# Optimization experiments

Hardware: AMD Instinct MI355X
Metric: run time of the kernel (lower is better)

## Reference

```python
import jax, jax.numpy as jnp
import numpy as np

N, L, DV, EF = 64, 128, 16, 4
D, H, FF, LC, K, MS = 256, 8, 1024, 3, 6, 16
DK = D // H
NEG = -1e9


def _ln(x, g, b):
    m = x.mean(-1, keepdims=True)
    v = ((x - m) ** 2).mean(-1, keepdims=True)
    return (x - m) / jnp.sqrt(v + 1e-5) * g + b


def setup_inputs() -> dict:
    key = jax.random.key(0)
    ks = jax.random.split(key, 20)
    s = 0.05
    rn = lambda k, sh: jax.random.normal(k, sh, jnp.float32) * s
    return {
        "vehicles": jax.random.normal(ks[0], (N, L, DV), jnp.float32),
        "fleet_edges": jax.random.uniform(ks[1], (N, L, L, EF), jnp.float32),
        "Wproj": rn(ks[2], (DV, D)), "bproj": jnp.zeros((D,), jnp.float32),
        "Wq": rn(ks[3], (LC, D, D)), "Wk": rn(ks[4], (LC, D, D)), "Wv": rn(ks[5], (LC, D, D)),
        "mix1_w": rn(ks[6], (LC, H, 2, MS)), "mix1_b": jnp.zeros((LC, H, MS), jnp.float32),
        "mix2_w": rn(ks[7], (LC, H, MS)), "mix2_b": jnp.zeros((LC, H), jnp.float32),
        "Wo": rn(ks[8], (LC, D, D)), "bo": jnp.zeros((LC, D), jnp.float32),
        "n1_g": jnp.ones((LC, D), jnp.float32), "n1_b": jnp.zeros((LC, D), jnp.float32),
        "ff1_w": rn(ks[9], (LC, D, FF)), "ff1_b": jnp.zeros((LC, FF), jnp.float32),
        "ff2_w": rn(ks[10], (LC, FF, D)), "ff2_b": jnp.zeros((LC, D), jnp.float32),
        "n2_g": jnp.ones((LC, D), jnp.float32), "n2_b": jnp.zeros((LC, D), jnp.float32),
    }


def _forward(vehicles, fleet_edges, Wproj, bproj, Wq, Wk, Wv, mix1_w, mix1_b,
             mix2_w, mix2_b, Wo, bo, n1_g, n1_b, ff1_w, ff1_b, ff2_w, ff2_b, n2_g, n2_b):
    h = vehicles @ Wproj + bproj                      # (N, L, D)
    dist = fleet_edges[..., 0]                        # (N, L, L)
    cost = dist
    # kNN mask: keep K smallest distances per row; mask==True -> blocked
    _, knn_idx = jax.lax.top_k(-dist, K)              # (N, L, K)
    nbr = jnp.any(jax.nn.one_hot(knn_idx, L, dtype=bool), axis=2)  # (N, L, L)
    mask = ~nbr
    row_fully_masked = mask.all(-1)                   # (N, L)
    inv_sqrt_dk = 1.0 / np.sqrt(DK).astype(np.float32)
    for i in range(LC):
        q = (h @ Wq[i]).reshape(N, L, H, DK).transpose(0, 2, 1, 3)
        k_ = (h @ Wk[i]).reshape(N, L, H, DK).transpose(0, 2, 1, 3)
        v = (h @ Wv[i]).reshape(N, L, H, DK).transpose(0, 2, 1, 3)
        dot = jnp.einsum('nhrd,nhcd->nhrc', q, k_) * inv_sqrt_dk      # (N,H,L,L)
        cost_b = jnp.broadcast_to(cost[:, None], (N, H, L, L))
        two = jnp.stack([dot, cost_b], axis=-1)                        # (N,H,L,L,2)
        ms1 = jax.nn.relu(jnp.einsum('nhrct,htm->nhrcm', two, mix1_w[i])
                          + mix1_b[i][None, :, None, None, :])         # (N,H,L,L,MS)
        score = jnp.einsum('nhrcm,hm->nhrc', ms1, mix2_w[i]) \
                + mix2_b[i][None, :, None, None]                       # (N,H,L,L)
        score = jnp.where(mask[:, None], NEG, score)
        w = jax.nn.softmax(score, axis=-1)
        att = jnp.einsum('nhrc,nhcd->nhrd', w, v)
        att = att.transpose(0, 2, 1, 3).reshape(N, L, D) @ Wo[i] + bo[i]
        h1 = _ln(h + att, n1_g[i], n1_b[i])
        ff = jax.nn.relu(h1 @ ff1_w[i] + ff1_b[i]) @ ff2_w[i] + ff2_b[i]
        h = _ln(h1 + ff, n2_g[i], n2_b[i])
        # original does h_out[mask] = 0; with kNN k>0 every row keeps k entries,
        # so only fully-masked rows would be zeroed (a no-op here, kept for fidelity)
        h = jnp.where(row_fully_masked[..., None], 0.0, h)
    return h


def reference(vehicles, fleet_edges, Wproj, bproj, Wq, Wk, Wv, mix1_w, mix1_b,
              mix2_w, mix2_b, Wo, bo, n1_g, n1_b, ff1_w, ff1_b, ff2_w, ff2_b, n2_g, n2_b):
    return _forward(vehicles, fleet_edges, Wproj, bproj, Wq, Wk, Wv, mix1_w, mix1_b,
                    mix2_w, mix2_b, Wo, bo, n1_g, n1_b, ff1_w, ff1_b, ff2_w, ff2_b, n2_g, n2_b)
```

## Files before the change

kernel.cpp:

```cpp
#include <hip/hip_runtime.h>
#include <math.h>

#define NB 64
#define LL 128
#define DV 16
#define DD 256
#define HH 8
#define DK 32
#define FF 1024
#define LC 3
#define KNN 6
#define MS 16
#define WLS 786432

typedef __attribute__((ext_vector_type(8))) short s16x8;
typedef __attribute__((ext_vector_type(4))) float f32x4;

static __device__ inline unsigned short f2b(float x) {
    union { float f; unsigned int u; } v; v.f = x;
    unsigned int r = (v.u + 0x7FFFu + ((v.u >> 16) & 1u)) >> 16;
    return (unsigned short)r;
}

static __device__ __forceinline__ void glds16(const void* g, void* l) {
    __builtin_amdgcn_global_load_lds(
        (const __attribute__((address_space(1))) void*)g,
        (__attribute__((address_space(3))) void*)l, 16, 0, 0);
}

__global__ __launch_bounds__(256)
void uber_pre(const float* __restrict__ veh, const float* __restrict__ Wp,
              const float* __restrict__ bp, float* __restrict__ h,
              unsigned short* __restrict__ hb,
              const float* __restrict__ edges, unsigned long long* __restrict__ idx8,
              const float* __restrict__ Wq, const float* __restrict__ Wk,
              const float* __restrict__ Wv, const float* __restrict__ Wo,
              const float* __restrict__ f1, const float* __restrict__ f2,
              unsigned short* __restrict__ Wt) {
    int bx = blockIdx.x;
    if (bx < 2048) {
        int m = bx * 4 + (threadIdx.x >> 6);
        int l = threadIdx.x & 63;
        int c0 = l * 4;
        const float4* w4 = reinterpret_cast<const float4*>(Wp);
        float4 a = *reinterpret_cast<const float4*>(bp + c0);
        const float* vr = veh + (size_t)m * DV;
#pragma unroll
        for (int t = 0; t < DV; ++t) {
            float vt = vr[t];
            float4 wv = w4[t * 64 + l];
            a.x += vt * wv.x; a.y += vt * wv.y; a.z += vt * wv.z; a.w += vt * wv.w;
        }
        *reinterpret_cast<float4*>(h + (size_t)m * DD + c0) = a;
        ushort4 u; u.x = f2b(a.x); u.y = f2b(a.y); u.z = f2b(a.z); u.w = f2b(a.w);
        *reinterpret_cast<ushort4*>(hb + (size_t)m * DD + c0) = u;
        return;
    }
    if (bx < 4096) {
        int row = (bx - 2048) * 4 + (threadIdx.x >> 6);
        int lane = threadIdx.x & 63;
        const float* dr = edges + (size_t)row * LL * 4;
        float v0 = dr[lane * 4], v1 = dr[(lane + 64) * 4];
        int i0 = lane, i1 = lane + 64;
        unsigned long long packed = 0;
#pragma unroll
        for (int k = 0; k < KNN; ++k) {
            float v; int i;
            if (v1 < v0) { v = v1; i = i1; } else { v = v0; i = i0; }
#pragma unroll
            for (int o = 1; o < 64; o <<= 1) {
                float ov = __shfl_xor(v, o);
                int oi = __shfl_xor(i, o);
                if (ov < v || (ov == v && oi < i)) { v = ov; i = oi; }
            }
            packed |= (unsigned long long)i << (k * 8);
            if (i == i0) v0 = 3.4e38f;
            if (i == i1) v1 = 3.4e38f;
        }
        if (lane == 0) idx8[row] = packed;
        return;
    }
    {
        int t = bx - 4096;
        int ll = t / 768, r = t % 768;
        int w, tile, K, N;
        if (r < 256)      { w = r >> 6; tile = r & 63;  K = DD; N = DD; }
        else if (r < 512) { w = 4; tile = r - 256;      K = DD; N = FF; }
        else              { w = 5; tile = r - 512;      K = FF; N = DD; }
        const float* src = (w == 0) ? Wq : (w == 1) ? Wk : (w == 2) ? Wv :
                           (w == 3) ? Wo : (w == 4) ? f1 : f2;
        src += (size_t)ll * K * N;
        long off = (w == 4) ? 262144L : (w == 5) ? 524288L : (long)w * 65536L;
        unsigned short* dst = Wt + (size_t)ll * WLS + off;
        int ntx = N >> 5;
        int n0 = (tile % ntx) * 32, k0 = (tile / ntx) * 32;
        int tx = threadIdx.x & 31, ty = threadIdx.x >> 5;
        __shared__ float T[32][33];
#pragma unroll
        for (int rr = 0; rr < 4; ++rr)
            T[ty + rr * 8][tx] = src[(size_t)(k0 + ty + rr * 8) * N + n0 + tx];
        __syncthreads();
#pragma unroll
        for (int rr = 0; rr < 4; ++rr)
            dst[(size_t)(n0 + ty + rr * 8) * K + k0 + tx] = f2b(T[tx][ty + rr * 8]);
    }
}

template <int BM, int BN, int WR, int WC, int MODE>
__global__ __launch_bounds__(256)
void gg(const unsigned short* __restrict__ A, const unsigned short* __restrict__ Bt,
        const float* __restrict__ bias, unsigned short* __restrict__ Cb,
        float* __restrict__ Oq, float* __restrict__ Ok, float* __restrict__ Ov,
        int K, int N) {
    constexpr int MI = BM / (WR * 16);
    constexpr int NJ = BN / (WC * 16);
    __shared__ unsigned short As[2][BM * 32];
    __shared__ unsigned short Bs[2][BN * 32];
    int tid = threadIdx.x;
    int w = tid >> 6, l = tid & 63;
    int lr = l & 15, lg = l >> 4;
    int wr = w % WR, wc = w / WR;
    int m0 = blockIdx.y * BM, n0 = blockIdx.x * BN;
    int row = tid >> 2, seg = tid & 3;

    auto STAGE = [&](int buf, int k0) {
#pragma unroll
        for (int r = 0; r < BM / 64; ++r)
            glds16(A + (size_t)(m0 + r * 64 + row) * K + k0 + seg * 8,
                   As[buf] + r * 2048 + w * 512);
#pragma unroll
        for (int r = 0; r < BN / 64; ++r)
            glds16(Bt + (size_t)(n0 + r * 64 + row) * K + k0 + seg * 8,
                   Bs[buf] + r * 2048 + w * 512);
    };

    f32x4 acc[MI][NJ];
#pragma unroll
    for (int i = 0; i < MI; ++i)
#pragma unroll
        for (int j = 0; j < NJ; ++j) acc[i][j] = (f32x4)(0.f);

    STAGE(0, 0);
    int nsteps = K >> 5;
    for (int step = 0; step < nsteps; ++step) {
        int cur = step & 1;
        __syncthreads();
        if (step + 1 < nsteps) STAGE(cur ^ 1, (step + 1) * 32);
        s16x8 af[MI], bf[NJ];
#pragma unroll
        for (int i = 0; i < MI; ++i)
            af[i] = *reinterpret_cast<const s16x8*>(
                As[cur] + (wr * MI * 16 + i * 16 + lr) * 32 + lg * 8);
#pragma unroll
        for (int j = 0; j < NJ; ++j)
            bf[j] = *reinterpret_cast<const s16x8*>(
                Bs[cur] + (wc * NJ * 16 + j * 16 + lr) * 32 + lg * 8);
#pragma unroll
        for (int i = 0; i < MI; ++i)
#pragma unroll
            for (int j = 0; j < NJ; ++j)
                acc[i][j] = __builtin_amdgcn_mfma_f32_16x16x32_bf16(af[i], bf[j], acc[i][j], 0, 0, 0);
    }

    if constexpr (MODE == 2) {
        int s = n0 >> 8;
        float* dst = (s == 0) ? Oq : (s == 1) ? Ok : Ov;
#pragma unroll
        for (int i = 0; i < MI; ++i)
#pragma unroll
            for (int j = 0; j < NJ; ++j) {
                int cc = (n0 & 255) + wc * NJ * 16 + j * 16 + lr;
                int hh = cc >> 5, dk = cc & 31;
                int grow = m0 + wr * MI * 16 + i * 16 + lg * 4;
                int nn = grow >> 7, rl = grow & 127;
                size_t ho = ((size_t)(nn * HH + hh) * LL + rl) * DK + dk;
#pragma unroll
                for (int q = 0; q < 4; ++q)
                    dst[ho + (size_t)q * DK] = acc[i][j][q];
            }
    } else {
#pragma unroll
        for (int i = 0; i < MI; ++i)
#pragma unroll
            for (int j = 0; j < NJ; ++j) {
                int col = n0 + wc * NJ * 16 + j * 16 + lr;
                float bc = bias[col];
#pragma unroll
                for (int q = 0; q < 4; ++q) {
                    int r = m0 + wr * MI * 16 + i * 16 + lg * 4 + q;
                    float v = fmaxf(acc[i][j][q] + bc, 0.f);
                    Cb[(size_t)r * N + col] = f2b(v);
                }
            }
    }
}

template <int KK, bool ATT>
__global__ __launch_bounds__(256)
void gg_ln(const unsigned short* __restrict__ A, const unsigned short* __restrict__ Bt,
           const float* __restrict__ qh, const float* __restrict__ kh,
           const float* __restrict__ vh, const float* __restrict__ edges,
           const unsigned long long* __restrict__ idx8,
           const float* __restrict__ m1w, const float* __restrict__ m1b,
           const float* __restrict__ m2w, const float* __restrict__ m2b,
           const float* __restrict__ bias, const float* __restrict__ res,
           const float* __restrict__ g, const float* __restrict__ be,
           float* __restrict__ out, unsigned short* __restrict__ outb) {
    __shared__ unsigned short Afull[ATT ? 16 * 264 : 1];
    __shared__ unsigned short As[ATT ? 1 : 2][16 * 32];
    __shared__ unsigned short Bs[2][256 * 32];
    __shared__ float Red[16][4];
    int tid = threadIdx.x;
    int w = tid >> 6, l = tid & 63;
    int lr = l & 15, lg = l >> 4;
    int m0 = blockIdx.x * 16;

    if constexpr (ATT) {
        int task = tid >> 1, sub = tid & 1;
        int rl = task & 15, hh = task >> 4;
        int n = m0 >> 7, r = (m0 & 127) + rl;
        int bh = n * HH + hh;
        const float scale = 0.17677669529663687f;
        const float* w0g = m1w + (hh * 2 + 0) * MS;
        const float* w1g = m1w + (hh * 2 + 1) * MS;
        const float* b1g = m1b + hh * MS;
        const float* w2g = m2w + hh * MS;
        float b2v = m2b[hh];

        const float4* qr = reinterpret_cast<const float4*>(
            qh + ((size_t)bh * LL + r) * DK) + sub * 4;
        float4 q[4];
#pragma unroll
        for (int j = 0; j < 4; ++j) q[j] = qr[j];

        unsigned long long pk = idx8[(size_t)n * LL + r];
        const float* kbase = kh + (size_t)bh * LL * DK;
        const float* vbase = vh + (size_t)bh * LL * DK;
        const float* erow = edges + (size_t)(n * LL + r) * LL * 4;

        int col[KNN];
#pragma unroll
        for (int k = 0; k < KNN; ++k) col[k] = (int)((pk >> (k * 8)) & 0xFF);

        float e[KNN];
        float mx = -3.4e38f;
#pragma unroll
        for (int k = 0; k < KNN; ++k) {
            const float4* kr = reinterpret_cast<const float4*>(
                kbase + (size_t)col[k] * DK) + sub * 4;
            float d = 0.f;
#pragma unroll
            for (int j = 0; j < 4; ++j) {
                float4 kv = kr[j];
                d += q[j].x * kv.x + q[j].y * kv.y + q[j].z * kv.z + q[j].w * kv.w;
            }
            d += __shfl_xor(d, 1);
            d *= scale;
            float cst = erow[col[k] * 4];
            float s = b2v;
#pragma unroll
            for (int m = 0; m < MS; ++m)
                s += fmaxf(d * w0g[m] + cst * w1g[m] + b1g[m], 0.f) * w2g[m];
            e[k] = s;
            mx = fmaxf(mx, s);
        }
        float sum = 0.f;
#pragma unroll
        for (int k = 0; k < KNN; ++k) { e[k] = __expf(e[k] - mx); sum += e[k]; }
        float inv = 1.f / sum;

        float4 att[4];
#pragma unroll
        for (int j = 0; j < 4; ++j) att[j] = make_float4(0.f, 0.f, 0.f, 0.f);
#pragma unroll
        for (int k = 0; k < KNN; ++k) {
            float wgt = e[k] * inv;
            const float4* vr = reinterpret_cast<const float4*>(
                vbase + (size_t)col[k] * DK) + sub * 4;
#pragma unroll
            for (int j = 0; j < 4; ++j) {
                float4 vv = vr[j];
                att[j].x += wgt * vv.x; att[j].y += wgt * vv.y;
                att[j].z += wgt * vv.z; att[j].w += wgt * vv.w;
            }
        }
        unsigned short* arow = Afull + rl * 264 + hh * DK + sub * 16;
#pragma unroll
        for (int j = 0; j < 4; ++j) {
            ushort4 u;
            u.x = f2b(att[j].x); u.y = f2b(att[j].y);
            u.z = f2b(att[j].z); u.w = f2b(att[j].w);
            *reinterpret_cast<ushort4*>(arow + j * 4) = u;
        }
    }

    auto STAGE = [&](int buf, int k0) {
        if constexpr (!ATT) {
            if (w == 0)
                glds16(A + (size_t)(m0 + (l >> 2)) * KK + k0 + (l & 3) * 8, As[buf]);
        }
#pragma unroll
        for (int i = 0; i < 4; ++i) {
            int idx = w * 4 + i;
            glds16(Bt + (size_t)(idx * 16 + (l >> 2)) * KK + k0 + (l & 3) * 8,
                   Bs[buf] + idx * 512);
        }
    };

    f32x4 acc[4];
#pragma unroll
    for (int j = 0; j < 4; ++j) acc[j] = (f32x4)(0.f);

    STAGE(0, 0);
    constexpr int NSTEPS = KK >> 5;
    for (int step = 0; step < NSTEPS; ++step) {
        int cur = step & 1;
        __syncthreads();
        if (step + 1 < NSTEPS) STAGE(cur ^ 1, (step + 1) * 32);
        s16x8 af;
        if constexpr (ATT)
            af = *reinterpret_cast<const s16x8*>(Afull + lr * 264 + step * 32 + lg * 8);
        else
            af = *reinterpret_cast<const s16x8*>(As[cur] + lr * 32 + lg * 8);
#pragma unroll
        for (int j = 0; j < 4; ++j) {
            s16x8 bf = *reinterpret_cast<const s16x8*>(
                Bs[cur] + (w * 64 + j * 16 + lr) * 32 + lg * 8);
            acc[j] = __builtin_amdgcn_mfma_f32_16x16x32_bf16(af, bf, acc[j], 0, 0, 0);
        }
    }

    float rsum[4] = {0.f, 0.f, 0.f, 0.f};
#pragma unroll
    for (int j = 0; j < 4; ++j) {
        int col = w * 64 + j * 16 + lr;
        float bc = bias[col];
#pragma unroll
        for (int q = 0; q < 4; ++q) {
            float x = acc[j][q] + bc + res[(size_t)(m0 + lg * 4 + q) * DD + col];
            acc[j][q] = x;
            rsum[q] += x;
        }
    }
#pragma unroll
    for (int q = 0; q < 4; ++q)
#pragma unroll
        for (int o = 1; o < 16; o <<= 1) rsum[q] += __shfl_xor(rsum[q], o);
    __syncthreads();
    if (lr == 0)
#pragma unroll
        for (int q = 0; q < 4; ++q) Red[lg * 4 + q][w] = rsum[q];
    __syncthreads();
    float mean[4];
#pragma unroll
    for (int q = 0; q < 4; ++q) {
        int row = lg * 4 + q;
        mean[q] = (Red[row][0] + Red[row][1] + Red[row][2] + Red[row][3]) * (1.0f / 256.0f);
    }
    float ssum[4] = {0.f, 0.f, 0.f, 0.f};
#pragma unroll
    for (int j = 0; j < 4; ++j)
#pragma unroll
        for (int q = 0; q < 4; ++q) {
            float d = acc[j][q] - mean[q];
            ssum[q] += d * d;
        }
#pragma unroll
    for (int q = 0; q < 4; ++q)
#pragma unroll
        for (int o = 1; o < 16; o <<= 1) ssum[q] += __shfl_xor(ssum[q], o);
    __syncthreads();
    if (lr == 0)
#pragma unroll
        for (int q = 0; q < 4; ++q) Red[lg * 4 + q][w] = ssum[q];
    __syncthreads();
    float rstd[4];
#pragma unroll
    for (int q = 0; q < 4; ++q) {
        int row = lg * 4 + q;
        float var = (Red[row][0] + Red[row][1] + Red[row][2] + Red[row][3]) * (1.0f / 256.0f);
        rstd[q] = 1.0f / sqrtf(var + 1e-5f);
    }
#pragma unroll
    for (int j = 0; j < 4; ++j) {
        int col = w * 64 + j * 16 + lr;
        float gc = g[col], bc2 = be[col];
#pragma unroll
        for (int q = 0; q < 4; ++q) {
            size_t off = (size_t)(m0 + lg * 4 + q) * DD + col;
            float v = (acc[j][q] - mean[q]) * rstd[q] * gc + bc2;
            out[off] = v;
            outb[off] = f2b(v);
        }
    }
}

extern "C" void kernel_launch(void* const* d_in, const int* in_sizes, int n_in,
                              void* d_out, int out_size, void* d_ws, size_t ws_size,
                              hipStream_t stream) {
    const float* vehicles = (const float*)d_in[0];
    const float* fleet    = (const float*)d_in[1];
    const float* Wproj    = (const float*)d_in[2];
    const float* bproj    = (const float*)d_in[3];
    const float* Wq       = (const float*)d_in[4];
    const float* Wk       = (const float*)d_in[5];
    const float* Wv       = (const float*)d_in[6];
    const float* m1w      = (const float*)d_in[7];
    const float* m1b      = (const float*)d_in[8];
    const float* m2w      = (const float*)d_in[9];
    const float* m2b      = (const float*)d_in[10];
    const float* Wo       = (const float*)d_in[11];
    const float* bo       = (const float*)d_in[12];
    const float* n1_g     = (const float*)d_in[13];
    const float* n1_b     = (const float*)d_in[14];
    const float* ff1_w    = (const float*)d_in[15];
    const float* ff1_b    = (const float*)d_in[16];
    const float* ff2_w    = (const float*)d_in[17];
    const float* ff2_b    = (const float*)d_in[18];
    const float* n2_g     = (const float*)d_in[19];
    const float* n2_b     = (const float*)d_in[20];

    const size_t MROWS = (size_t)NB * LL;
    const size_t HSZ   = MROWS * DD;

    float* ws = (float*)d_ws;
    float* h   = ws;
    float* qh  = h + HSZ;
    float* kh  = qh + HSZ;
    float* vh  = kh + HSZ;
    unsigned short* hb    = (unsigned short*)(vh + HSZ);
    unsigned short* ffmid = hb + HSZ;
    unsigned short* Wt    = ffmid + MROWS * FF;
    unsigned long long* idx8 = (unsigned long long*)(Wt + 3 * WLS);

    uber_pre<<<6400, 256, 0, stream>>>(vehicles, Wproj, bproj, h, hb,
                                       fleet, idx8,
                                       Wq, Wk, Wv, Wo, ff1_w, ff2_w, Wt);

    dim3 gqkv(12, 128);
    dim3 gff1(8, 128);

    for (int i = 0; i < LC; ++i) {
        const unsigned short* wt = Wt + (size_t)i * WLS;

        gg<64, 64, 2, 2, 2><<<gqkv, 256, 0, stream>>>(
            hb, wt, nullptr, nullptr, qh, kh, vh, DD, 768);

        gg_ln<256, true><<<512, 256, 0, stream>>>(
            nullptr, wt + 196608,
            qh, kh, vh, fleet, idx8,
            m1w + (size_t)i * HH * 2 * MS, m1b + (size_t)i * HH * MS,
            m2w + (size_t)i * HH * MS,     m2b + (size_t)i * HH,
            bo + (size_t)i * DD,
            h, n1_g + (size_t)i * DD, n1_b + (size_t)i * DD, h, hb);

        gg<64, 128, 2, 2, 1><<<gff1, 256, 0, stream>>>(
            hb, wt + 262144, ff1_b + (size_t)i * FF, ffmid,
            nullptr, nullptr, nullptr, DD, FF);

        float* dst = (i == LC - 1) ? (float*)d_out : h;
        gg_ln<1024, false><<<512, 256, 0, stream>>>(
            ffmid, wt + 524288,
            nullptr, nullptr, nullptr, nullptr, nullptr,
            nullptr, nullptr, nullptr, nullptr,
            ff2_b + (size_t)i * DD,
            h, n2_g + (size_t)i * DD, n2_b + (size_t)i * DD, dst, hb);
    }
}
```

Before: 227.7 us.

## Fuse FF1 and FF2 with layernorm into one per-row-block kernel

Replaces the separate FF1 GEMM kernel and the FF2+layernorm kernel with a single kernel. Each 16-row block computes the ReLU FF1 output into shared memory (16x1024 bf16), then runs FF2, the residual add and the layernorm from it. This removes the global round trip of the intermediate activation and one launch per layer. The cost is that each block streams all of W1 and W2 with only 16 rows of reuse, on 512 blocks of 4 warps, so weight traffic per block rises and parallelism in the FF1 stage drops.

Result: slower. 243.1 us (+6.8%).

```diff
diff --git a/kernel.cpp b/kernel.cpp
--- a/kernel.cpp
+++ b/kernel.cpp
@@ -195,19 +195,18 @@
     }
 }
 
-template <int KK, bool ATT>
 __global__ __launch_bounds__(256)
-void gg_ln(const unsigned short* __restrict__ A, const unsigned short* __restrict__ Bt,
-           const float* __restrict__ qh, const float* __restrict__ kh,
-           const float* __restrict__ vh, const float* __restrict__ edges,
-           const unsigned long long* __restrict__ idx8,
-           const float* __restrict__ m1w, const float* __restrict__ m1b,
-           const float* __restrict__ m2w, const float* __restrict__ m2b,
-           const float* __restrict__ bias, const float* __restrict__ res,
-           const float* __restrict__ g, const float* __restrict__ be,
-           float* __restrict__ out, unsigned short* __restrict__ outb) {
-    __shared__ unsigned short Afull[ATT ? 16 * 264 : 1];
-    __shared__ unsigned short As[ATT ? 1 : 2][16 * 32];
+void attnwo_ln(const unsigned short* __restrict__ Bt,
+               const float* __restrict__ qh, const float* __restrict__ kh,
+               const float* __restrict__ vh, const float* __restrict__ edges,
+               const unsigned long long* __restrict__ idx8,
+               const float* __restrict__ m1w, const float* __restrict__ m1b,
+               const float* __restrict__ m2w, const float* __restrict__ m2b,
+               const float* __restrict__ bias, const float* __restrict__ res,
+               const float* __restrict__ g, const float* __restrict__ be,
+               float* __restrict__ out, unsigned short* __restrict__ outb) {
+    constexpr int KK = 256;
+    __shared__ unsigned short Afull[16 * 264];
     __shared__ unsigned short Bs[2][256 * 32];
     __shared__ float Red[16][4];
     int tid = threadIdx.x;
@@ -215,7 +214,7 @@
     int lr = l & 15, lg = l >> 4;
     int m0 = blockIdx.x * 16;
 
-    if constexpr (ATT) {
+    {
         int task = tid >> 1, sub = tid & 1;
         int rl = task & 15, hh = task >> 4;
         int n = m0 >> 7, r = (m0 & 127) + rl;
@@ -295,10 +294,6 @@
     }
 
     auto STAGE = [&](int buf, int k0) {
-        if constexpr (!ATT) {
-            if (w == 0)
-                glds16(A + (size_t)(m0 + (l >> 2)) * KK + k0 + (l & 3) * 8, As[buf]);
-        }
 #pragma unroll
         for (int i = 0; i < 4; ++i) {
             int idx = w * 4 + i;
@@ -317,11 +312,7 @@
         int cur = step & 1;
         __syncthreads();
         if (step + 1 < NSTEPS) STAGE(cur ^ 1, (step + 1) * 32);
-        s16x8 af;
-        if constexpr (ATT)
-            af = *reinterpret_cast<const s16x8*>(Afull + lr * 264 + step * 32 + lg * 8);
-        else
-            af = *reinterpret_cast<const s16x8*>(As[cur] + lr * 32 + lg * 8);
+        s16x8 af = *reinterpret_cast<const s16x8*>(Afull + lr * 264 + step * 32 + lg * 8);
 #pragma unroll
         for (int j = 0; j < 4; ++j) {
             s16x8 bf = *reinterpret_cast<const s16x8*>(
@@ -335,6 +326,158 @@
     for (int j = 0; j < 4; ++j) {
         int col = w * 64 + j * 16 + lr;
         float bc = bias[col];
+#pragma unroll
+        for (int q = 0; q < 4; ++q) {
+            float x = acc[j][q] + bc + res[(size_t)(m0 + lg * 4 + q) * DD + col];
+            acc[j][q] = x;
+            rsum[q] += x;
+        }
+    }
+#pragma unroll
+    for (int q = 0; q < 4; ++q)
+#pragma unroll
+        for (int o = 1; o < 16; o <<= 1) rsum[q] += __shfl_xor(rsum[q], o);
+    __syncthreads();
+    if (lr == 0)
+#pragma unroll
+        for (int q = 0; q < 4; ++q) Red[lg * 4 + q][w] = rsum[q];
+    __syncthreads();
+    float mean[4];
+#pragma unroll
+    for (int q = 0; q < 4; ++q) {
+        int row = lg * 4 + q;
+        mean[q] = (Red[row][0] + Red[row][1] + Red[row][2] + Red[row][3]) * (1.0f / 256.0f);
+    }
+    float ssum[4] = {0.f, 0.f, 0.f, 0.f};
+#pragma unroll
+    for (int j = 0; j < 4; ++j)
+#pragma unroll
+        for (int q = 0; q < 4; ++q) {
+            float d = acc[j][q] - mean[q];
+            ssum[q] += d * d;
+        }
+#pragma unroll
+    for (int q = 0; q < 4; ++q)
+#pragma unroll
+        for (int o = 1; o < 16; o <<= 1) ssum[q] += __shfl_xor(ssum[q], o);
+    __syncthreads();
+    if (lr == 0)
+#pragma unroll
+        for (int q = 0; q < 4; ++q) Red[lg * 4 + q][w] = ssum[q];
+    __syncthreads();
+    float rstd[4];
+#pragma unroll
+    for (int q = 0; q < 4; ++q) {
+        int row = lg * 4 + q;
+        float var = (Red[row][0] + Red[row][1] + Red[row][2] + Red[row][3]) * (1.0f / 256.0f);
+        rstd[q] = 1.0f / sqrtf(var + 1e-5f);
+    }
+#pragma unroll
+    for (int j = 0; j < 4; ++j) {
+        int col = w * 64 + j * 16 + lr;
+        float gc = g[col], bc2 = be[col];
+#pragma unroll
+        for (int q = 0; q < 4; ++q) {
+            size_t off = (size_t)(m0 + lg * 4 + q) * DD + col;
+            float v = (acc[j][q] - mean[q]) * rstd[q] * gc + bc2;
+            out[off] = v;
+            outb[off] = f2b(v);
+        }
+    }
+}
+
+__global__ __launch_bounds__(256)
+void ff_ln(const unsigned short* __restrict__ hb_in,
+           const unsigned short* __restrict__ W1t, const unsigned short* __restrict__ W2t,
+           const float* __restrict__ b1, const float* __restrict__ b2,
+           const float* __restrict__ res, const float* __restrict__ g,
+           const float* __restrict__ be,
+           float* __restrict__ out, unsigned short* __restrict__ outb) {
+    __shared__ unsigned short fm[16 * 1032];
+    __shared__ unsigned short Bs[2][256 * 32];
+    __shared__ float Red[16][4];
+    int tid = threadIdx.x;
+    int w = tid >> 6, l = tid & 63;
+    int lr = l & 15, lg = l >> 4;
+    int m0 = blockIdx.x * 16;
+
+    s16x8 af1[8];
+    {
+        const unsigned short* arow = hb_in + (size_t)(m0 + lr) * DD + lg * 8;
+#pragma unroll
+        for (int s = 0; s < 8; ++s)
+            af1[s] = *reinterpret_cast<const s16x8*>(arow + s * 32);
+    }
+
+    auto STAGE1 = [&](int buf, int stage) {
+        int chunk = stage >> 3, k0 = (stage & 7) * 32;
+        const unsigned short* base = W1t + (size_t)(chunk * 256) * DD;
+#pragma unroll
+        for (int i = 0; i < 4; ++i) {
+            int idx = w * 4 + i;
+            glds16(base + (size_t)(idx * 16 + (l >> 2)) * DD + k0 + (l & 3) * 8,
+                   Bs[buf] + idx * 512);
+        }
+    };
+    auto STAGE2 = [&](int buf, int step) {
+        int k0 = step * 32;
+#pragma unroll
+        for (int i = 0; i < 4; ++i) {
+            int idx = w * 4 + i;
+            glds16(W2t + (size_t)(idx * 16 + (l >> 2)) * FF + k0 + (l & 3) * 8,
+                   Bs[buf] + idx * 512);
+        }
+    };
+
+    f32x4 acc[4];
+#pragma unroll
+    for (int j = 0; j < 4; ++j) acc[j] = (f32x4)(0.f);
+
+    STAGE1(0, 0);
+    for (int stage = 0; stage < 32; ++stage) {
+        int cur = stage & 1;
+        __syncthreads();
+        if (stage + 1 < 32) STAGE1(cur ^ 1, stage + 1);
+        else               STAGE2(cur ^ 1, 0);
+        s16x8 af = af1[stage & 7];
+#pragma unroll
+        for (int j = 0; j < 4; ++j) {
+            s16x8 bf = *reinterpret_cast<const s16x8*>(
+                Bs[cur] + (w * 64 + j * 16 + lr) * 32 + lg * 8);
+            acc[j] = __builtin_amdgcn_mfma_f32_16x16x32_bf16(af, bf, acc[j], 0, 0, 0);
+        }
+        if ((stage & 7) == 7) {
+            int nc = stage >> 3;
+#pragma unroll
+            for (int j = 0; j < 4; ++j) {
+                int col = nc * 256 + w * 64 + j * 16 + lr;
+                float bc = b1[col];
+#pragma unroll
+                for (int q = 0; q < 4; ++q)
+                    fm[(lg * 4 + q) * 1032 + col] = f2b(fmaxf(acc[j][q] + bc, 0.f));
+                acc[j] = (f32x4)(0.f);
+            }
+        }
+    }
+
+    for (int step = 0; step < 32; ++step) {
+        int cur = step & 1;
+        __syncthreads();
+        if (step + 1 < 32) STAGE2(cur ^ 1, step + 1);
+        s16x8 af = *reinterpret_cast<const s16x8*>(fm + lr * 1032 + step * 32 + lg * 8);
+#pragma unroll
+        for (int j = 0; j < 4; ++j) {
+            s16x8 bf = *reinterpret_cast<const s16x8*>(
+                Bs[cur] + (w * 64 + j * 16 + lr) * 32 + lg * 8);
+            acc[j] = __builtin_amdgcn_mfma_f32_16x16x32_bf16(af, bf, acc[j], 0, 0, 0);
+        }
+    }
+
+    float rsum[4] = {0.f, 0.f, 0.f, 0.f};
+#pragma unroll
+    for (int j = 0; j < 4; ++j) {
+        int col = w * 64 + j * 16 + lr;
+        float bc = b2[col];
 #pragma unroll
         for (int q = 0; q < 4; ++q) {
             float x = acc[j][q] + bc + res[(size_t)(m0 + lg * 4 + q) * DD + col];
@@ -428,9 +571,8 @@
     float* qh  = h + HSZ;
     float* kh  = qh + HSZ;
     float* vh  = kh + HSZ;
-    unsigned short* hb    = (unsigned short*)(vh + HSZ);
-    unsigned short* ffmid = hb + HSZ;
-    unsigned short* Wt    = ffmid + MROWS * FF;
+    unsigned short* hb = (unsigned short*)(vh + HSZ);
+    unsigned short* Wt = hb + HSZ;
     unsigned long long* idx8 = (unsigned long long*)(Wt + 3 * WLS);
 
     uber_pre<<<6400, 256, 0, stream>>>(vehicles, Wproj, bproj, h, hb,
@@ -438,7 +580,6 @@
                                        Wq, Wk, Wv, Wo, ff1_w, ff2_w, Wt);
 
     dim3 gqkv(12, 128);
-    dim3 gff1(8, 128);
 
     for (int i = 0; i < LC; ++i) {
         const unsigned short* wt = Wt + (size_t)i * WLS;
@@ -446,24 +587,18 @@
         gg<64, 64, 2, 2, 2><<<gqkv, 256, 0, stream>>>(
             hb, wt, nullptr, nullptr, qh, kh, vh, DD, 768);
 
-        gg_ln<256, true><<<512, 256, 0, stream>>>(
-            nullptr, wt + 196608,
+        attnwo_ln<<<512, 256, 0, stream>>>(
+            wt + 196608,
             qh, kh, vh, fleet, idx8,
             m1w + (size_t)i * HH * 2 * MS, m1b + (size_t)i * HH * MS,
             m2w + (size_t)i * HH * MS,     m2b + (size_t)i * HH,
             bo + (size_t)i * DD,
             h, n1_g + (size_t)i * DD, n1_b + (size_t)i * DD, h, hb);
 
-        gg<64, 128, 2, 2, 1><<<gff1, 256, 0, stream>>>(
-            hb, wt + 262144, ff1_b + (size_t)i * FF, ffmid,
-            nullptr, nullptr, nullptr, DD, FF);
-
         float* dst = (i == LC - 1) ? (float*)d_out : h;
-        gg_ln<1024, false><<<512, 256, 0, stream>>>(
-            ffmid, wt + 524288,
-            nullptr, nullptr, nullptr, nullptr, nullptr,
-            nullptr, nullptr, nullptr, nullptr,
-            ff2_b + (size_t)i * DD,
+        ff_ln<<<512, 256, 0, stream>>>(
+            hb, wt + 262144, wt + 524288,
+            ff1_b + (size_t)i * FF, ff2_b + (size_t)i * DD,
             h, n2_g + (size_t)i * DD, n2_b + (size_t)i * DD, dst, hb);
     }
 }
```
